# Optimization experiments

Hardware: AMD Instinct MI355X
Metric: run time of the kernel (lower is better)

The kernel has to match this reference:

```python
import jax, jax.numpy as jnp
import numpy as np

SEQ = 8192
D_IN = 1024
D_OUT = 128


def setup_inputs() -> dict:
    key = jax.random.key(0)
    k0, k1, k2, k3 = jax.random.split(key, 4)
    # kaiming-normal-ish init for weights (std = sqrt(2/fan_in))
    std = np.sqrt(2.0 / D_IN).astype(np.float32)
    return {
        "x": jax.random.normal(k0, (SEQ, D_IN), dtype=jnp.float32),
        "wq": jax.random.normal(k1, (D_IN, D_OUT), dtype=jnp.float32) * std,
        "wk": jax.random.normal(k2, (D_IN, D_OUT), dtype=jnp.float32) * std,
        "wv": jax.random.normal(k3, (D_IN, D_OUT), dtype=jnp.float32) * std,
    }


def reference(x, wq, wk, wv):
    # q,k,v: [S, d_out]
    q = x @ wq
    k = x @ wk
    v = x @ wv
    scale = jnp.sqrt(jnp.asarray(D_OUT, dtype=q.dtype))
    scores = (q @ k.T) / scale          # [S, S]
    attn = jax.nn.softmax(scores, axis=-1)
    return attn @ v                      # [S, d_out]
```

## Files before the change

### kernel.cpp

```cpp
#include <hip/hip_runtime.h>
#include <cstdint>

#define SEQ    8192
#define DIN    1024
#define DOUT   128
#define NSPLIT 8
#define KVTILE 32
#define QTILE  64
#define QK_SCALE 0.1275174246f

typedef unsigned short u16;
typedef __bf16 bf16x8 __attribute__((ext_vector_type(8)));
typedef float  f32x4  __attribute__((ext_vector_type(4)));
typedef float  f32x16 __attribute__((ext_vector_type(16)));
typedef unsigned short u16x8 __attribute__((ext_vector_type(8)));
typedef unsigned short u16x4 __attribute__((ext_vector_type(4)));
typedef unsigned int u32x2 __attribute__((ext_vector_type(2)));
typedef unsigned int u32x4 __attribute__((ext_vector_type(4)));

__device__ __forceinline__ u16 bfc(float f) {
  return __builtin_bit_cast(u16, (__bf16)f);
}
__device__ __forceinline__ float bf2f(u16 u) {
  union { uint32_t u; float f; } c; c.u = ((uint32_t)u) << 16; return c.f;
}

__device__ __forceinline__ bf16x8 ldsu8(const u16* base, int byteoff) {
  return __builtin_bit_cast(bf16x8,
    *reinterpret_cast<const u16x8*>(reinterpret_cast<const char*>(base) + byteoff));
}
__device__ __forceinline__ bf16x8 glbu8(const u16* p) {
  return __builtin_bit_cast(bf16x8, *reinterpret_cast<const u16x8*>(p));
}

__device__ __forceinline__ void gload_lds16(const void* g, void* l) {
  __builtin_amdgcn_global_load_lds(
      (const __attribute__((address_space(1))) void*)g,
      (__attribute__((address_space(3))) void*)l, 16, 0, 0);
}

__global__ __launch_bounds__(256) void k_wtrans(const float* __restrict__ wq,
                                                const float* __restrict__ wk,
                                                const float* __restrict__ wv,
                                                u16* __restrict__ Wt) {
  const float* w = (blockIdx.y == 0) ? wq : (blockIdx.y == 1) ? wk : wv;
  int idx = blockIdx.x * 256 + threadIdx.x;
  int k = idx >> 7, n = idx & 127;
  Wt[(size_t)blockIdx.y * (DOUT * DIN) + (size_t)n * DIN + k] = bfc(w[idx]);
}

__global__ __launch_bounds__(256) void k_xcast(const float* __restrict__ x,
                                               u16* __restrict__ Xb) {
  size_t base = ((size_t)blockIdx.x * 256 + threadIdx.x) * 8;
  float4 lo = *reinterpret_cast<const float4*>(x + base);
  float4 hi = *reinterpret_cast<const float4*>(x + base + 4);
  u16x8 v = { bfc(lo.x), bfc(lo.y), bfc(lo.z), bfc(lo.w),
              bfc(hi.x), bfc(hi.y), bfc(hi.z), bfc(hi.w) };
  *reinterpret_cast<u16x8*>(Xb + base) = v;
}

__global__ __launch_bounds__(256, 2) void k_gemm(const u16* __restrict__ Xb,
                                                 const u16* __restrict__ Wt,
                                                 u16* __restrict__ Q,
                                                 u16* __restrict__ K,
                                                 u16* __restrict__ Vt) {
  __shared__ __attribute__((aligned(16))) u16 As[2][64 * 128];
  __shared__ __attribute__((aligned(16))) u16 Bs[2][96 * 128];
  const int tid  = threadIdx.x;
  const int lane = tid & 63, wave = tid >> 6;
  const int lm   = lane & 15, g = lane >> 4;
  const int wm   = wave >> 1, wn = wave & 1;
  const int m0   = blockIdx.x * 64;
  const int n0   = blockIdx.y * 96;
  const int swzr = (lm & 7) << 4;

  const int trow = tid >> 4;
  const int tswz = ((tid & 15) << 4) ^ ((trow & 7) << 4);
  const char* baseA = (const char*)Xb + (size_t)(m0 + trow) * 2048 + tswz;
  const char* baseB = (const char*)Wt + (size_t)(n0 + trow) * 2048 + tswz;

  auto stage = [&](int buf, int kc) {
    const int kb = kc * 256;
#pragma unroll
    for (int i = 0; i < 4; ++i)
      gload_lds16(baseA + kb + i * 32768, &As[buf][i * 2048 + wave * 512]);
#pragma unroll
    for (int j = 0; j < 6; ++j)
      gload_lds16(baseB + kb + j * 32768, &Bs[buf][j * 2048 + wave * 512]);
  };

  f32x4 acc[2][3];
#pragma unroll
  for (int s = 0; s < 2; ++s)
#pragma unroll
    for (int nb = 0; nb < 3; ++nb) acc[s][nb] = (f32x4){0.f, 0.f, 0.f, 0.f};

  auto compute = [&](int buf) {
    const u16* As_ = As[buf];
    const u16* Bs_ = Bs[buf];
    bf16x8 a[2][4], b[3][4];
#pragma unroll
    for (int s = 0; s < 2; ++s)
#pragma unroll
      for (int t = 0; t < 4; ++t)
        a[s][t] = ldsu8(As_, (wm * 32 + s * 16 + lm) * 256 +
                             ((t * 64 + 16 * g) ^ swzr));
#pragma unroll
    for (int nb = 0; nb < 3; ++nb)
#pragma unroll
      for (int t = 0; t < 4; ++t)
        b[nb][t] = ldsu8(Bs_, (wn * 48 + nb * 16 + lm) * 256 +
                              ((t * 64 + 16 * g) ^ swzr));
#pragma unroll
    for (int s = 0; s < 2; ++s)
#pragma unroll
      for (int nb = 0; nb < 3; ++nb)
#pragma unroll
        for (int t = 0; t < 4; ++t)
          acc[s][nb] = __builtin_amdgcn_mfma_f32_16x16x32_bf16(
              a[s][t], b[nb][t], acc[s][nb], 0, 0, 0);
  };

  stage(0, 0);
  asm volatile("s_waitcnt vmcnt(0)" ::: "memory");
  __syncthreads();

#pragma unroll
  for (int kc = 0; kc < 8; kc += 2) {
    if (kc + 1 < 8) stage(1, kc + 1);
    compute(0);
    asm volatile("s_waitcnt vmcnt(0)" ::: "memory");
    __syncthreads();
    if (kc + 2 < 8) stage(0, kc + 2);
    compute(1);
    asm volatile("s_waitcnt vmcnt(0)" ::: "memory");
    __syncthreads();
  }

#pragma unroll
  for (int s = 0; s < 2; ++s)
#pragma unroll
    for (int nb = 0; nb < 3; ++nb) {
      int n = n0 + wn * 48 + nb * 16 + lm;
      int which = n >> 7, col = n & 127;
#pragma unroll
      for (int r = 0; r < 4; ++r) {
        int m = m0 + wm * 32 + s * 16 + g * 4 + r;
        if (which == 0)       Q[(size_t)m * DOUT + col] = bfc(acc[s][nb][r] * QK_SCALE);
        else if (which == 1)  K[(size_t)m * DOUT + col] = bfc(acc[s][nb][r]);
        else                  Vt[(size_t)col * SEQ + m] = bfc(acc[s][nb][r]);
      }
    }
}

__global__ __launch_bounds__(128, 2) void k_attn(const u16* __restrict__ Q,
                                                 const u16* __restrict__ K,
                                                 const u16* __restrict__ Vt,
                                                 u16* __restrict__ Op,
                                                 float* __restrict__ Lb) {
  __shared__ __attribute__((aligned(16))) u16 Ks[2][32 * 128];
  __shared__ __attribute__((aligned(16))) u16 Vts[3][128 * 32];
  const int tid  = threadIdx.x;
  const int lane = tid & 63, wave = tid >> 6;
  const int l31  = lane & 31, h = lane >> 5;
  const int bid  = blockIdx.x;
  const int split = bid & 7;
  const int m0   = (bid >> 3) * QTILE;
  const int kvbase = split * (SEQ / NSPLIT);
  const int NIT = (SEQ / NSPLIT) / KVTILE;

  auto stageK = [&](int kb, int kv0) {
#pragma unroll
    for (int i = 0; i < 4; ++i) {
      int krow = wave * 16 + i * 4 + (lane >> 4);
      const char* gk = (const char*)K + ((size_t)(kv0 + krow) << 8) +
                       (((lane & 15) << 4) ^ ((krow & 7) << 4));
      gload_lds16(gk, &Ks[kb][wave * 2048 + i * 512]);
    }
  };
  auto stageV = [&](u16* vbuf, int kv0) {
#pragma unroll
    for (int i = 0; i < 4; ++i) {
      int vrow = wave * 64 + i * 16 + (lane >> 2);
      const char* gv = (const char*)Vt + (size_t)vrow * (SEQ * 2) +
                       (size_t)kv0 * 2 +
                       (((lane & 3) << 4) ^ (((vrow >> 1) & 3) << 4));
      gload_lds16(gv, vbuf + wave * 2048 + i * 512);
    }
  };

  bf16x8 qf[8];

  f32x16 o[4] = {};
  float lr = 0.f;

  auto qk = [&](const u16* ks) -> f32x16 {
    f32x16 a0 = {}, a1 = {};
    const int rswz = (l31 & 7) << 4;
#pragma unroll
    for (int t = 0; t < 8; t += 2) {
      bf16x8 k0 = ldsu8(ks, l31 * 256 + ((t * 32 + 16 * h) ^ rswz));
      bf16x8 k1 = ldsu8(ks, l31 * 256 + (((t + 1) * 32 + 16 * h) ^ rswz));
      a0 = __builtin_amdgcn_mfma_f32_32x32x16_bf16(k0, qf[t], a0, 0, 0, 0);
      a1 = __builtin_amdgcn_mfma_f32_32x32x16_bf16(k1, qf[t + 1], a1, 0, 0, 0);
    }
    return a0 + a1;
  };

  auto smpv = [&](f32x16 s, const u16* vs) {
    float rsum = 0.f;
#pragma unroll
    for (int j = 0; j < 2; ++j) {
      const int base = j * 8;
      float e0 = exp2f(s[base + 0]);
      float e1 = exp2f(s[base + 1]);
      float e2 = exp2f(s[base + 2]);
      float e3 = exp2f(s[base + 3]);
      float e4 = exp2f(s[base + 4]);
      float e5 = exp2f(s[base + 5]);
      float e6 = exp2f(s[base + 6]);
      float e7 = exp2f(s[base + 7]);
      rsum += ((e0 + e1) + (e2 + e3)) + ((e4 + e5) + (e6 + e7));
      u16x4 wa = { bfc(e0), bfc(e1), bfc(e2), bfc(e3) };
      u16x4 wb = { bfc(e4), bfc(e5), bfc(e6), bfc(e7) };
      u32x2 A = __builtin_bit_cast(u32x2, wa);
      u32x2 B = __builtin_bit_cast(u32x2, wb);
      u32x2 r01 = __builtin_amdgcn_permlane32_swap(A.x, B.x, false, false);
      u32x2 r23 = __builtin_amdgcn_permlane32_swap(A.y, B.y, false, false);
      u32x4 fr = { r01.x, r23.x, r01.y, r23.y };
      bf16x8 pb = __builtin_bit_cast(bf16x8, fr);
#pragma unroll
      for (int db = 0; db < 4; ++db) {
        int vrow = db * 32 + l31;
        bf16x8 vb = ldsu8(vs, vrow * 64 +
                              ((32 * j + 16 * h) ^ (((vrow >> 1) & 3) << 4)));
        o[db] = __builtin_amdgcn_mfma_f32_32x32x16_bf16(vb, pb, o[db], 0, 0, 0);
      }
    }
    lr += rsum;
  };

  u16 *vA = Vts[0], *vB = Vts[1], *vC = Vts[2];
  stageK(0, kvbase);
  stageV(vA, kvbase);
  stageK(1, kvbase + KVTILE);
  stageV(vB, kvbase + KVTILE);
  {
    const u16* qp = Q + (size_t)(m0 + wave * 32 + l31) * DOUT + 8 * h;
#pragma unroll
    for (int t = 0; t < 8; ++t) qf[t] = glbu8(qp + t * 16);
  }
  asm volatile("s_waitcnt vmcnt(0)" ::: "memory");
  __syncthreads();
  f32x16 sA = qk(Ks[0]);
  f32x16 sB;

  for (int t = 0; t < NIT; t += 2) {
    const bool more = (t + 2 < NIT);
    if (more) asm volatile("s_waitcnt vmcnt(4) lgkmcnt(0)" ::: "memory");
    else      asm volatile("s_waitcnt vmcnt(0) lgkmcnt(0)" ::: "memory");
    __builtin_amdgcn_s_barrier();
    if (more) {
      stageK(0, kvbase + (t + 2) * KVTILE);
      stageV(vC, kvbase + (t + 2) * KVTILE);
    }
    sB = qk(Ks[1]);
    smpv(sA, vA);
    { u16* tp = vA; vA = vB; vB = vC; vC = tp; }

    if (more) asm volatile("s_waitcnt vmcnt(4) lgkmcnt(0)" ::: "memory");
    else      asm volatile("s_waitcnt vmcnt(0) lgkmcnt(0)" ::: "memory");
    __builtin_amdgcn_s_barrier();
    if (t + 3 < NIT) {
      stageK(1, kvbase + (t + 3) * KVTILE);
      stageV(vC, kvbase + (t + 3) * KVTILE);
    }
    if (more) sA = qk(Ks[0]);
    smpv(sB, vA);
    { u16* tp = vA; vA = vB; vB = vC; vC = tp; }
  }

  lr += __shfl_xor(lr, 32);

  const size_t ob = (size_t)split * SEQ * DOUT;
  const int q = m0 + wave * 32 + l31;
#pragma unroll
  for (int db = 0; db < 4; ++db)
#pragma unroll
    for (int j = 0; j < 4; ++j) {
      u16x4 w = { bfc(o[db][4 * j + 0]), bfc(o[db][4 * j + 1]),
                  bfc(o[db][4 * j + 2]), bfc(o[db][4 * j + 3]) };
      *reinterpret_cast<u16x4*>(Op + ob + (size_t)q * DOUT +
                                db * 32 + 8 * j + 4 * h) = w;
    }
  if (h == 0) Lb[split * SEQ + q] = lr;
}

__global__ __launch_bounds__(256) void k_combine(const u16* __restrict__ Op,
                                                 const float* __restrict__ Lb,
                                                 float* __restrict__ out) {
  int idx = blockIdx.x * 256 + threadIdx.x;
  int srow = idx >> 7;
  float num = 0.f, den = 0.f;
  const size_t st = (size_t)SEQ * DOUT;
#pragma unroll
  for (int s = 0; s < NSPLIT; ++s) {
    den += Lb[s * SEQ + srow];
    num += bf2f(Op[s * st + idx]);
  }
  out[idx] = num / den;
}

extern "C" void kernel_launch(void* const* d_in, const int* in_sizes, int n_in,
                              void* d_out, int out_size, void* d_ws, size_t ws_size,
                              hipStream_t stream) {
  const float* x  = (const float*)d_in[0];
  const float* wq = (const float*)d_in[1];
  const float* wk = (const float*)d_in[2];
  const float* wv = (const float*)d_in[3];
  char* ws = (char*)d_ws;

  const size_t MB = (size_t)1 << 20;
  u16*   Wt = (u16*)(ws);
  u16*   Q  = (u16*)(ws + 768 * 1024);
  u16*   K  = (u16*)(ws + 768 * 1024 + 2 * MB);
  u16*   Vt = (u16*)(ws + 768 * 1024 + 4 * MB);
  float* Lb = (float*)(ws + 768 * 1024 + 6 * MB + 256 * 1024);
  u16*   Xb = (u16*)(ws + 7 * MB + 256 * 1024);
  u16*   Op = (u16*)(ws + 7 * MB + 256 * 1024);
  float* out = (float*)d_out;

  k_wtrans<<<dim3((DIN * DOUT) / 256, 3), 256, 0, stream>>>(wq, wk, wv, Wt);
  k_xcast<<<dim3((SEQ * DIN) / (256 * 8)), 256, 0, stream>>>(x, Xb);
  k_gemm<<<dim3(SEQ / 64, 4), 256, 0, stream>>>(Xb, Wt, Q, K, Vt);
  k_attn<<<dim3((SEQ / QTILE) * NSPLIT), 128, 0, stream>>>(Q, K, Vt, Op, Lb);
  k_combine<<<dim3((SEQ * DOUT) / 256), 256, 0, stream>>>(Op, Lb, out);
}
```

Before: 90.11 us.

## Fuse fp32-to-bf16 cast of x into GEMM staging and vectorize combine

Removes the separate x cast kernel. The GEMM now loads fp32 x rows into registers, converts them to bf16 and writes them into the swizzled LDS tile after the compute step, overlapping the conversion with MFMA work. This avoids writing and rereading a bf16 copy of x and saves one launch, but each of the four column blocks now reads the fp32 x, doubling per-read bytes. The combine kernel is also vectorized to process eight elements per thread with a reciprocal multiply.

Measured after the change: 86.72 us, median of 2. 3.8% less time.

```diff
diff --git a/kernel.cpp b/kernel.cpp
--- a/kernel.cpp
+++ b/kernel.cpp
@@ -49,17 +49,7 @@
   Wt[(size_t)blockIdx.y * (DOUT * DIN) + (size_t)n * DIN + k] = bfc(w[idx]);
 }
 
-__global__ __launch_bounds__(256) void k_xcast(const float* __restrict__ x,
-                                               u16* __restrict__ Xb) {
-  size_t base = ((size_t)blockIdx.x * 256 + threadIdx.x) * 8;
-  float4 lo = *reinterpret_cast<const float4*>(x + base);
-  float4 hi = *reinterpret_cast<const float4*>(x + base + 4);
-  u16x8 v = { bfc(lo.x), bfc(lo.y), bfc(lo.z), bfc(lo.w),
-              bfc(hi.x), bfc(hi.y), bfc(hi.z), bfc(hi.w) };
-  *reinterpret_cast<u16x8*>(Xb + base) = v;
-}
-
-__global__ __launch_bounds__(256, 2) void k_gemm(const u16* __restrict__ Xb,
+__global__ __launch_bounds__(256, 2) void k_gemm(const float* __restrict__ x,
                                                  const u16* __restrict__ Wt,
                                                  u16* __restrict__ Q,
                                                  u16* __restrict__ K,
@@ -74,19 +64,31 @@
   const int n0   = blockIdx.y * 96;
   const int swzr = (lm & 7) << 4;
 
+  const int arow = tid >> 2, acol = tid & 3;
+  const float* xbase = x + (size_t)(m0 + arow) * DIN + acol * 4;
   const int trow = tid >> 4;
   const int tswz = ((tid & 15) << 4) ^ ((trow & 7) << 4);
-  const char* baseA = (const char*)Xb + (size_t)(m0 + trow) * 2048 + tswz;
   const char* baseB = (const char*)Wt + (size_t)(n0 + trow) * 2048 + tswz;
 
-  auto stage = [&](int buf, int kc) {
+  float4 fa[8];
+  auto stage_load = [&](int bbuf, int kc) {
+    const float* xp = xbase + kc * 128;
+#pragma unroll
+    for (int i = 0; i < 8; ++i)
+      fa[i] = *reinterpret_cast<const float4*>(xp + i * 16);
     const int kb = kc * 256;
 #pragma unroll
-    for (int i = 0; i < 4; ++i)
-      gload_lds16(baseA + kb + i * 32768, &As[buf][i * 2048 + wave * 512]);
-#pragma unroll
     for (int j = 0; j < 6; ++j)
-      gload_lds16(baseB + kb + j * 32768, &Bs[buf][j * 2048 + wave * 512]);
+      gload_lds16(baseB + kb + j * 32768, &Bs[bbuf][j * 2048 + wave * 512]);
+  };
+  auto stage_write = [&](int abuf) {
+    char* dst = reinterpret_cast<char*>(As[abuf]) + arow * 256;
+    const int sw = (arow & 7) << 4;
+#pragma unroll
+    for (int i = 0; i < 8; ++i) {
+      u16x4 w = { bfc(fa[i].x), bfc(fa[i].y), bfc(fa[i].z), bfc(fa[i].w) };
+      *reinterpret_cast<u16x4*>(dst + ((acol * 8 + i * 32) ^ sw)) = w;
+    }
   };
 
   f32x4 acc[2][3];
@@ -121,18 +123,21 @@
               a[s][t], b[nb][t], acc[s][nb], 0, 0, 0);
   };
 
-  stage(0, 0);
+  stage_load(0, 0);
+  stage_write(0);
   asm volatile("s_waitcnt vmcnt(0)" ::: "memory");
   __syncthreads();
 
 #pragma unroll
   for (int kc = 0; kc < 8; kc += 2) {
-    if (kc + 1 < 8) stage(1, kc + 1);
+    if (kc + 1 < 8) stage_load(1, kc + 1);
     compute(0);
+    if (kc + 1 < 8) stage_write(1);
     asm volatile("s_waitcnt vmcnt(0)" ::: "memory");
     __syncthreads();
-    if (kc + 2 < 8) stage(0, kc + 2);
+    if (kc + 2 < 8) stage_load(0, kc + 2);
     compute(1);
+    if (kc + 2 < 8) stage_write(0);
     asm volatile("s_waitcnt vmcnt(0)" ::: "memory");
     __syncthreads();
   }
@@ -299,16 +304,23 @@
 __global__ __launch_bounds__(256) void k_combine(const u16* __restrict__ Op,
                                                  const float* __restrict__ Lb,
                                                  float* __restrict__ out) {
-  int idx = blockIdx.x * 256 + threadIdx.x;
-  int srow = idx >> 7;
-  float num = 0.f, den = 0.f;
+  int e0 = (blockIdx.x * 256 + threadIdx.x) * 8;
+  int srow = e0 >> 7;
+  float den = 0.f;
+  float acc[8] = {};
   const size_t st = (size_t)SEQ * DOUT;
 #pragma unroll
   for (int s = 0; s < NSPLIT; ++s) {
     den += Lb[s * SEQ + srow];
-    num += bf2f(Op[s * st + idx]);
+    u16x8 v = *reinterpret_cast<const u16x8*>(Op + s * st + e0);
+#pragma unroll
+    for (int i = 0; i < 8; ++i) acc[i] += bf2f(v[i]);
   }
-  out[idx] = num / den;
+  float r = 1.f / den;
+  float4 o0 = { acc[0] * r, acc[1] * r, acc[2] * r, acc[3] * r };
+  float4 o1 = { acc[4] * r, acc[5] * r, acc[6] * r, acc[7] * r };
+  *reinterpret_cast<float4*>(out + e0) = o0;
+  *reinterpret_cast<float4*>(out + e0 + 4) = o1;
 }
 
 extern "C" void kernel_launch(void* const* d_in, const int* in_sizes, int n_in,
@@ -326,13 +338,11 @@
   u16*   K  = (u16*)(ws + 768 * 1024 + 2 * MB);
   u16*   Vt = (u16*)(ws + 768 * 1024 + 4 * MB);
   float* Lb = (float*)(ws + 768 * 1024 + 6 * MB + 256 * 1024);
-  u16*   Xb = (u16*)(ws + 7 * MB + 256 * 1024);
   u16*   Op = (u16*)(ws + 7 * MB + 256 * 1024);
   float* out = (float*)d_out;
 
   k_wtrans<<<dim3((DIN * DOUT) / 256, 3), 256, 0, stream>>>(wq, wk, wv, Wt);
-  k_xcast<<<dim3((SEQ * DIN) / (256 * 8)), 256, 0, stream>>>(x, Xb);
-  k_gemm<<<dim3(SEQ / 64, 4), 256, 0, stream>>>(Xb, Wt, Q, K, Vt);
+  k_gemm<<<dim3(SEQ / 64, 4), 256, 0, stream>>>(x, Wt, Q, K, Vt);
   k_attn<<<dim3((SEQ / QTILE) * NSPLIT), 128, 0, stream>>>(Q, K, Vt, Op, Lb);
-  k_combine<<<dim3((SEQ * DOUT) / 256), 256, 0, stream>>>(Op, Lb, out);
-}
+  k_combine<<<dim3((SEQ * DOUT) / (256 * 8)), 256, 0, stream>>>(Op, Lb, out);
+}
```
